# Kernel optimization log

Measured on AMD Instinct MI355X. Metric: run time of the kernel, lower is better.

## Reference

```python
import jax, jax.numpy as jnp
import numpy as np

N = 8192
D_IN = 512
D_OUT = 256
ALPHA = 0.2
NEG = -9e15


def setup_inputs() -> dict:
    key = jax.random.key(0)
    k1, k2, k3, k4 = jax.random.split(key, 4)
    node = jax.random.normal(k1, (N, D_IN), dtype=jnp.float32)
    adj = jax.random.randint(k2, (N, N), 0, 2, dtype=jnp.int32)
    # xavier_uniform with gain=1.414
    gain = 1.414
    lim_w = gain * np.sqrt(6.0 / (D_IN + D_OUT))
    weight = jax.random.uniform(k3, (D_IN, D_OUT), minval=-lim_w, maxval=lim_w, dtype=jnp.float32)
    lim_a = gain * np.sqrt(6.0 / (2 * D_OUT + 1))
    a = jax.random.uniform(k4, (2 * D_OUT, 1), minval=-lim_a, maxval=lim_a, dtype=jnp.float32)
    bias = jnp.zeros((D_OUT,), dtype=jnp.float32)
    return {"node": node, "adj": adj, "weight": weight, "a": a, "bias": bias}


def reference(node, adj, weight, a, bias):
    # v: [N, D_OUT]
    v = node @ weight
    # per-node attention scalars: Q, K are [N, 1]
    Q = v @ a[:D_OUT, :]
    K = v @ a[D_OUT:, :]
    e = jax.nn.leaky_relu(Q + K.T, negative_slope=ALPHA)  # [N, N]
    attention = jnp.where(adj > 0, e, NEG)
    attention = jax.nn.softmax(attention, axis=1)
    # dropout is identity in eval mode (self.training == False)
    out = attention @ v  # [N, D_OUT]
    out = jax.nn.leaky_relu(out, negative_slope=ALPHA)
    # F.normalize(p=2, dim=1): x / max(||x||_2, 1e-12)
    norm = jnp.linalg.norm(out, axis=1, keepdims=True)
    out = out / jnp.maximum(norm, 1e-12)
    return out + bias
```

## Files before the change

### kernel.cpp

```cpp
#include <hip/hip_runtime.h>
#include <hip/hip_bf16.h>

#define N_NODES 8192
#define DIN     512
#define DOUT    256
#define ALPHA   0.2f
#define LOG2E   1.4426950408889634f

typedef __bf16 bf16x8 __attribute__((ext_vector_type(8)));
typedef __bf16 bf16x4 __attribute__((ext_vector_type(4)));
typedef float  f32x4  __attribute__((ext_vector_type(4)));
typedef int    i32x4  __attribute__((ext_vector_type(4)));
typedef unsigned u32x4 __attribute__((ext_vector_type(4)));

__global__ __launch_bounds__(256) void k_repack_w(const float* __restrict__ w,
                                                  bf16x8* __restrict__ wB,
                                                  unsigned* __restrict__ kmaxkey) {
    if (blockIdx.x == 0 && threadIdx.x == 0) *kmaxkey = 0u;
    int u = blockIdx.x * 256 + threadIdx.x;
    int lane = u & 63, t = u >> 6;
    int nt = t & 15, kt = t >> 4;
    int k0 = kt * 32 + (lane >> 4) * 8;
    int col = nt * 16 + (lane & 15);
    bf16x8 r;
#pragma unroll
    for (int i = 0; i < 8; ++i) r[i] = (__bf16)w[(size_t)(k0 + i) * DOUT + col];
    wB[u] = r;
}

__global__ __launch_bounds__(256) void k_gemm1f(const float* __restrict__ node,
                                                const bf16x8* __restrict__ wB,
                                                const float* __restrict__ a,
                                                bf16x8* __restrict__ vBo,
                                                float* __restrict__ Q, float* __restrict__ K,
                                                unsigned* __restrict__ kmaxkey) {
    __shared__ __bf16 vsh[32][260];
    __shared__ float qksh[32][2];
    int lane = threadIdx.x & 63, w = threadIdx.x >> 6;
    int r15 = lane & 15, g = lane >> 4;
    int nh = w & 1, rh = w >> 1;
    int rowbase = blockIdx.x * 32;
    int myrow = rowbase + rh * 16 + r15;
    const float* np = node + (size_t)myrow * DIN + g * 8;

    f32x4 acc[8];
#pragma unroll
    for (int j = 0; j < 8; ++j) acc[j] = (f32x4){0.f, 0.f, 0.f, 0.f};

    f32x4 c0 = *(const f32x4*)np;
    f32x4 c1 = *(const f32x4*)(np + 4);
    f32x4 c2 = *(const f32x4*)(np + 32);
    f32x4 c3 = *(const f32x4*)(np + 36);
    const bf16x8* wp = wB + (size_t)(nh * 8) * 64 + lane;
    bf16x8 fr0 = wp[0], fr1 = wp[64], fr2 = wp[128], fr3 = wp[192];
    bf16x8 fr4 = wp[256], fr5 = wp[320], fr6 = wp[384], fr7 = wp[448];

    for (int kt = 0; kt < 16; ++kt) {
        f32x4 u0 = c0, u1 = c1;
        c0 = c2; c1 = c3;
        if (kt + 2 < 16) {
            c2 = *(const f32x4*)(np + (kt + 2) * 32);
            c3 = *(const f32x4*)(np + (kt + 2) * 32 + 4);
        }
        bf16x8 f0 = fr0, f1 = fr1, f2 = fr2, f3 = fr3;
        bf16x8 f4 = fr4, f5 = fr5, f6 = fr6, f7 = fr7;
        if (kt + 1 < 16) {
            const bf16x8* wn = wB + ((size_t)(kt + 1) * 16 + nh * 8) * 64 + lane;
            fr0 = wn[0]; fr1 = wn[64]; fr2 = wn[128]; fr3 = wn[192];
            fr4 = wn[256]; fr5 = wn[320]; fr6 = wn[384]; fr7 = wn[448];
        }
        bf16x8 af;
#pragma unroll
        for (int i = 0; i < 4; ++i) { af[i] = (__bf16)u0[i]; af[i + 4] = (__bf16)u1[i]; }
        acc[0] = __builtin_amdgcn_mfma_f32_16x16x32_bf16(af, f0, acc[0], 0, 0, 0);
        acc[1] = __builtin_amdgcn_mfma_f32_16x16x32_bf16(af, f1, acc[1], 0, 0, 0);
        acc[2] = __builtin_amdgcn_mfma_f32_16x16x32_bf16(af, f2, acc[2], 0, 0, 0);
        acc[3] = __builtin_amdgcn_mfma_f32_16x16x32_bf16(af, f3, acc[3], 0, 0, 0);
        acc[4] = __builtin_amdgcn_mfma_f32_16x16x32_bf16(af, f4, acc[4], 0, 0, 0);
        acc[5] = __builtin_amdgcn_mfma_f32_16x16x32_bf16(af, f5, acc[5], 0, 0, 0);
        acc[6] = __builtin_amdgcn_mfma_f32_16x16x32_bf16(af, f6, acc[6], 0, 0, 0);
        acc[7] = __builtin_amdgcn_mfma_f32_16x16x32_bf16(af, f7, acc[7], 0, 0, 0);
    }

    float qp0 = 0.f, qp1 = 0.f, qp2 = 0.f, qp3 = 0.f;
    float kp0 = 0.f, kp1 = 0.f, kp2 = 0.f, kp3 = 0.f;
#pragma unroll
    for (int j = 0; j < 8; ++j) {
        int col = (nh * 8 + j) * 16 + r15;
        float a1 = a[col], a2 = a[DOUT + col];
        qp0 += acc[j][0] * a1; qp1 += acc[j][1] * a1;
        qp2 += acc[j][2] * a1; qp3 += acc[j][3] * a1;
        kp0 += acc[j][0] * a2; kp1 += acc[j][1] * a2;
        kp2 += acc[j][2] * a2; kp3 += acc[j][3] * a2;
    }
#pragma unroll
    for (int m = 1; m < 16; m <<= 1) {
        qp0 += __shfl_xor(qp0, m); qp1 += __shfl_xor(qp1, m);
        qp2 += __shfl_xor(qp2, m); qp3 += __shfl_xor(qp3, m);
        kp0 += __shfl_xor(kp0, m); kp1 += __shfl_xor(kp1, m);
        kp2 += __shfl_xor(kp2, m); kp3 += __shfl_xor(kp3, m);
    }

#pragma unroll
    for (int j = 0; j < 8; ++j)
#pragma unroll
        for (int r = 0; r < 4; ++r)
            vsh[rh * 16 + g * 4 + r][(nh * 8 + j) * 16 + r15] = (__bf16)acc[j][r];
    if (nh == 0 && r15 == 0) {
        int rl = rh * 16 + g * 4;
        qksh[rl + 0][0] = qp0; qksh[rl + 1][0] = qp1; qksh[rl + 2][0] = qp2; qksh[rl + 3][0] = qp3;
        qksh[rl + 0][1] = kp0; qksh[rl + 1][1] = kp1; qksh[rl + 2][1] = kp2; qksh[rl + 3][1] = kp3;
    }
    __syncthreads();
    if (nh == 1 && r15 == 0) {
        int rl = rh * 16 + g * 4;
        int rw = rowbase + rl;
        float q0 = qp0 + qksh[rl + 0][0], q1 = qp1 + qksh[rl + 1][0];
        float q2 = qp2 + qksh[rl + 2][0], q3 = qp3 + qksh[rl + 3][0];
        float k0 = kp0 + qksh[rl + 0][1], k1 = kp1 + qksh[rl + 1][1];
        float k2 = kp2 + qksh[rl + 2][1], k3 = kp3 + qksh[rl + 3][1];
        Q[rw + 0] = q0; Q[rw + 1] = q1; Q[rw + 2] = q2; Q[rw + 3] = q3;
        K[rw + 0] = k0; K[rw + 1] = k1; K[rw + 2] = k2; K[rw + 3] = k3;
        float km = fmaxf(fmaxf(k0, k1), fmaxf(k2, k3));
        unsigned bits = __float_as_uint(km);
        unsigned key = (bits & 0x80000000u) ? ~bits : (bits | 0x80000000u);
        atomicMax(kmaxkey, key);
    }
#pragma unroll
    for (int uu = 0; uu < 4; ++uu) {
        int nt = w * 4 + uu;
        bf16x8 t;
#pragma unroll
        for (int i = 0; i < 8; ++i) t[i] = vsh[g * 8 + i][nt * 16 + r15];
        vBo[((size_t)blockIdx.x * 16 + nt) * 64 + lane] = t;
    }
}

template<int JS>
__global__ __launch_bounds__(256) void k_attn(const int* __restrict__ adj,
                                              const bf16x8* __restrict__ vBg,
                                              const float* __restrict__ Q,
                                              const float* __restrict__ K,
                                              const unsigned* __restrict__ kmaxkey,
                                              __bf16* __restrict__ accB,
                                              float* __restrict__ Sp) {
    constexpr int JR   = N_NODES / JS;
    constexpr int BIT  = JR / 32;
    constexpr int MSTR = BIT + 4;
    __shared__ float    Ks[JR];
    __shared__ unsigned Ms[64][MSTR];
    __shared__ bf16x8   pT[2][4][64];

    int bid = blockIdx.x;
    int rb = bid / JS, p = bid % JS;
    int lane = threadIdx.x & 63, w = threadIdx.x >> 6;
    int r15 = lane & 15, g = lane >> 4;
    int rowbase = rb * 64;
    int prow = rowbase + w * 16 + r15;
    int j0 = p * JR;

    for (int s = threadIdx.x * 4; s < JR; s += 1024)
        *(f32x4*)&Ks[s] = *(const f32x4*)&K[j0 + s];

    {
        const int t = threadIdx.x;
#pragma unroll
        for (int s = 0; s < BIT / 4; ++s) {
            int task = s * 256 + t;
            int row = task / BIT, dcol = task % BIT;
            const int* src = adj + (size_t)(rowbase + row) * N_NODES + j0 + dcol * 32;
            unsigned m = 0;
#pragma unroll
            for (int q = 0; q < 8; ++q) {
                i32x4 av = *(const i32x4*)(src + q * 4);
                m |= (av[0] != 0 ? 1u : 0u) << (q * 4 + 0);
                m |= (av[1] != 0 ? 1u : 0u) << (q * 4 + 1);
                m |= (av[2] != 0 ? 1u : 0u) << (q * 4 + 2);
                m |= (av[3] != 0 ? 1u : 0u) << (q * 4 + 3);
            }
            Ms[row][dcol] = m;
        }
    }

    float qi = Q[prow];
    unsigned kk = *kmaxkey;
    unsigned kb = (kk & 0x80000000u) ? (kk ^ 0x80000000u) : ~kk;
    float kmax = __uint_as_float(kb);
    float t0 = qi + kmax;
    float c2 = fmaxf(t0, ALPHA * t0) * LOG2E;

    const bf16x8* vbp = vBg + ((size_t)(p * BIT) * 16 + w * 4) * 64 + lane;

    f32x4 acc[4][4];
#pragma unroll
    for (int m = 0; m < 4; ++m)
#pragma unroll
        for (int n = 0; n < 4; ++n) acc[m][n] = (f32x4){0.f, 0.f, 0.f, 0.f};
    float sl = 0.f;

    __syncthreads();

    u32x4 Wc = *(const u32x4*)&Ms[w * 16 + r15][0];
    bf16x8 vS0 = vbp[0],    vS1 = vbp[64],   vS2 = vbp[128],  vS3 = vbp[192];
    bf16x8 vT0 = vbp[1024], vT1 = vbp[1088], vT2 = vbp[1152], vT3 = vbp[1216];

#define BODYM(W32, V0, V1, V2, V3, BUF, itv)                                    \
    {                                                                           \
        bf16x8 b0 = V0, b1 = V1, b2 = V2, b3 = V3;                              \
        if ((itv) + 2 < BIT) {                                                  \
            V0 = vbp[((itv) + 2) * 1024];       V1 = vbp[((itv) + 2) * 1024 + 64];  \
            V2 = vbp[((itv) + 2) * 1024 + 128]; V3 = vbp[((itv) + 2) * 1024 + 192]; \
        }                                                                       \
        f32x4 q0 = *(const f32x4*)&Ks[(itv) * 32 + g * 8];                      \
        f32x4 q1 = *(const f32x4*)&Ks[(itv) * 32 + g * 8 + 4];                  \
        unsigned wsh = (W32) >> (g * 8);                                        \
        bf16x8 af;                                                              \
        _Pragma("unroll")                                                       \
        for (int i = 0; i < 8; ++i) {                                           \
            float kj = (i < 4) ? q0[i] : q1[i - 4];                             \
            float tt = qi + kj;                                                 \
            float ft = fmaxf(tt, ALPHA * tt);                                   \
            float pv = __builtin_amdgcn_exp2f(ft * LOG2E - c2);                 \
            pv = (wsh & (1u << i)) ? pv : 0.f;                                  \
            sl += pv;                                                           \
            af[i] = (__bf16)pv;                                                 \
        }                                                                       \
        pT[BUF][w][lane] = af;                                                  \
        asm volatile("s_waitcnt lgkmcnt(0)" ::: "memory");                      \
        __builtin_amdgcn_s_barrier();                                           \
        asm volatile("" ::: "memory");                                          \
        bf16x8 pa0 = pT[BUF][0][lane], pa1 = pT[BUF][1][lane];                  \
        bf16x8 pa2 = pT[BUF][2][lane], pa3 = pT[BUF][3][lane];                  \
        acc[0][0] = __builtin_amdgcn_mfma_f32_16x16x32_bf16(pa0, b0, acc[0][0], 0, 0, 0); \
        acc[0][1] = __builtin_amdgcn_mfma_f32_16x16x32_bf16(pa0, b1, acc[0][1], 0, 0, 0); \
        acc[0][2] = __builtin_amdgcn_mfma_f32_16x16x32_bf16(pa0, b2, acc[0][2], 0, 0, 0); \
        acc[0][3] = __builtin_amdgcn_mfma_f32_16x16x32_bf16(pa0, b3, acc[0][3], 0, 0, 0); \
        acc[1][0] = __builtin_amdgcn_mfma_f32_16x16x32_bf16(pa1, b0, acc[1][0], 0, 0, 0); \
        acc[1][1] = __builtin_amdgcn_mfma_f32_16x16x32_bf16(pa1, b1, acc[1][1], 0, 0, 0); \
        acc[1][2] = __builtin_amdgcn_mfma_f32_16x16x32_bf16(pa1, b2, acc[1][2], 0, 0, 0); \
        acc[1][3] = __builtin_amdgcn_mfma_f32_16x16x32_bf16(pa1, b3, acc[1][3], 0, 0, 0); \
        acc[2][0] = __builtin_amdgcn_mfma_f32_16x16x32_bf16(pa2, b0, acc[2][0], 0, 0, 0); \
        acc[2][1] = __builtin_amdgcn_mfma_f32_16x16x32_bf16(pa2, b1, acc[2][1], 0, 0, 0); \
        acc[2][2] = __builtin_amdgcn_mfma_f32_16x16x32_bf16(pa2, b2, acc[2][2], 0, 0, 0); \
        acc[2][3] = __builtin_amdgcn_mfma_f32_16x16x32_bf16(pa2, b3, acc[2][3], 0, 0, 0); \
        acc[3][0] = __builtin_amdgcn_mfma_f32_16x16x32_bf16(pa3, b0, acc[3][0], 0, 0, 0); \
        acc[3][1] = __builtin_amdgcn_mfma_f32_16x16x32_bf16(pa3, b1, acc[3][1], 0, 0, 0); \
        acc[3][2] = __builtin_amdgcn_mfma_f32_16x16x32_bf16(pa3, b2, acc[3][2], 0, 0, 0); \
        acc[3][3] = __builtin_amdgcn_mfma_f32_16x16x32_bf16(pa3, b3, acc[3][3], 0, 0, 0); \
    }

    for (int it4 = 0; it4 < BIT; it4 += 4) {
        u32x4 Wn = Wc;
        if (it4 + 4 < BIT) Wn = *(const u32x4*)&Ms[w * 16 + r15][it4 + 4];
        BODYM(Wc[0], vS0, vS1, vS2, vS3, 0, it4 + 0)
        BODYM(Wc[1], vT0, vT1, vT2, vT3, 1, it4 + 1)
        BODYM(Wc[2], vS0, vS1, vS2, vS3, 0, it4 + 2)
        BODYM(Wc[3], vT0, vT1, vT2, vT3, 1, it4 + 3)
        Wc = Wn;
    }
#undef BODYM

    sl += __shfl_xor(sl, 16);
    sl += __shfl_xor(sl, 32);
    if (g == 0) Sp[(size_t)p * N_NODES + prow] = sl;

    __bf16* apb = accB + ((size_t)p * N_NODES + rowbase) * DOUT;
#pragma unroll
    for (int m = 0; m < 4; ++m)
#pragma unroll
        for (int r = 0; r < 4; ++r) {
            bf16x4 t;
#pragma unroll
            for (int n = 0; n < 4; ++n) t[n] = (__bf16)acc[m][n][r];
            *(bf16x4*)&apb[(size_t)(m * 16 + g * 4 + r) * DOUT + w * 64 + r15 * 4] = t;
        }
}

template<int JS>
__global__ __launch_bounds__(256) void k_final(const __bf16* __restrict__ accB,
                                               const float* __restrict__ Sp,
                                               const float* __restrict__ bias,
                                               float* __restrict__ out) {
    int lane = threadIdx.x & 63, wv = threadIdx.x >> 6;
    int row = blockIdx.x * 4 + wv;
    float s = 0.f;
    f32x4 av = (f32x4){0.f, 0.f, 0.f, 0.f};
#pragma unroll
    for (int pp = 0; pp < JS; ++pp) {
        bf16x4 t = *(const bf16x4*)&accB[((size_t)pp * N_NODES + row) * DOUT + lane * 4];
#pragma unroll
        for (int j = 0; j < 4; ++j) av[j] += (float)t[j];
        s += Sp[(size_t)pp * N_NODES + row];
    }
    float inv = 1.0f / fmaxf(s, 1e-30f);
    f32x4 o;
#pragma unroll
    for (int j = 0; j < 4; ++j) {
        float x = av[j] * inv;
        o[j] = fmaxf(x, ALPHA * x);
    }
    float sq = o[0] * o[0] + o[1] * o[1] + o[2] * o[2] + o[3] * o[3];
#pragma unroll
    for (int m = 1; m < 64; m <<= 1) sq += __shfl_xor(sq, m);
    float innrm = 1.0f / fmaxf(sqrtf(sq), 1e-12f);
#pragma unroll
    for (int j = 0; j < 4; ++j) {
        int col = (lane >> 4) * 64 + j * 16 + (lane & 15);
        out[(size_t)row * DOUT + col] = o[j] * innrm + bias[col];
    }
}

extern "C" void kernel_launch(void* const* d_in, const int* in_sizes, int n_in,
                              void* d_out, int out_size, void* d_ws, size_t ws_size,
                              hipStream_t stream) {
    const float* node   = (const float*)d_in[0];
    const int*   adj    = (const int*)d_in[1];
    const float* weight = (const float*)d_in[2];
    const float* a      = (const float*)d_in[3];
    const float* bias   = (const float*)d_in[4];
    float* out = (float*)d_out;

    const size_t fixed  = 4522240;
    const size_t per_js = 32768 + (size_t)N_NODES * DOUT * 2;
    int js = (ws_size >= fixed + 8 * per_js) ? 8 : 4;

    char* ws = (char*)d_ws;
    bf16x8*   wB      = (bf16x8*)(ws);
    bf16x8*   vB      = (bf16x8*)(ws + 262144);
    float*    Q       = (float*)(ws + 4456448);
    float*    K       = (float*)(ws + 4489216);
    unsigned* kmaxkey = (unsigned*)(ws + 4521984);
    float*    Sp      = (float*)(ws + fixed);
    __bf16*   accB    = (__bf16*)(ws + fixed + (size_t)js * 32768);

    k_repack_w<<<dim3(64),  dim3(256), 0, stream>>>(weight, wB, kmaxkey);
    k_gemm1f  <<<dim3(256), dim3(256), 0, stream>>>(node, wB, a, vB, Q, K, kmaxkey);
    if (js == 8) {
        k_attn<8><<<dim3(128 * 8), dim3(256), 0, stream>>>(adj, vB, Q, K, kmaxkey, accB, Sp);
        k_final<8><<<dim3(2048), dim3(256), 0, stream>>>(accB, Sp, bias, out);
    } else {
        k_attn<4><<<dim3(128 * 4), dim3(256), 0, stream>>>(adj, vB, Q, K, kmaxkey, accB, Sp);
        k_final<4><<<dim3(2048), dim3(256), 0, stream>>>(accB, Sp, bias, out);
    }
}
```

Baseline: 138.6 us.

## Stream adjacency bitmask packing into the attention main loop and simplify exp math

Instead of loading and packing the whole adjacency block into a shared-memory bitmask before the main loop, the kernel now packs only the first two column groups up front. Later groups are loaded and packed inside the loop two groups ahead, so the large int32 adjacency reads overlap with the exp and MFMA work. The leaky-relu plus exp argument is rewritten as a max of two FMAs with precomputed constants. Launch bounds now request two blocks per CU. This adds register pressure from the in-flight adjacency vectors, and the packing is only correct if NG is at least 3 and matches the four-threads-per-row mapping.

```diff
diff --git a/kernel.cpp b/kernel.cpp
--- a/kernel.cpp
+++ b/kernel.cpp
@@ -137,15 +137,16 @@
 }
 
 template<int JS>
-__global__ __launch_bounds__(256) void k_attn(const int* __restrict__ adj,
-                                              const bf16x8* __restrict__ vBg,
-                                              const float* __restrict__ Q,
-                                              const float* __restrict__ K,
-                                              const unsigned* __restrict__ kmaxkey,
-                                              __bf16* __restrict__ accB,
-                                              float* __restrict__ Sp) {
+__global__ __launch_bounds__(256, 2) void k_attn(const int* __restrict__ adj,
+                                                 const bf16x8* __restrict__ vBg,
+                                                 const float* __restrict__ Q,
+                                                 const float* __restrict__ K,
+                                                 const unsigned* __restrict__ kmaxkey,
+                                                 __bf16* __restrict__ accB,
+                                                 float* __restrict__ Sp) {
     constexpr int JR   = N_NODES / JS;
     constexpr int BIT  = JR / 32;
+    constexpr int NG   = BIT / 4;
     constexpr int MSTR = BIT + 4;
     __shared__ float    Ks[JR];
     __shared__ unsigned Ms[64][MSTR];
@@ -162,25 +163,28 @@
     for (int s = threadIdx.x * 4; s < JR; s += 1024)
         *(f32x4*)&Ks[s] = *(const f32x4*)&K[j0 + s];
 
+    const int t = threadIdx.x;
+    const int mrow = t >> 2, msub = t & 3;
+    const int* abase = adj + (size_t)(rowbase + mrow) * N_NODES + j0;
+
+#define ISSUE8(L, DC) { const int* src_ = abase + (DC) * 32;                     \
+    _Pragma("unroll") for (int q = 0; q < 8; ++q) L[q] = *(const i32x4*)(src_ + q * 4); }
+#define PACK32(L) ({ unsigned m_ = 0u;                                           \
+    _Pragma("unroll") for (int q = 0; q < 8; ++q) {                              \
+        m_ |= (L[q][0] != 0 ? 1u : 0u) << (q * 4 + 0);                           \
+        m_ |= (L[q][1] != 0 ? 1u : 0u) << (q * 4 + 1);                           \
+        m_ |= (L[q][2] != 0 ? 1u : 0u) << (q * 4 + 2);                           \
+        m_ |= (L[q][3] != 0 ? 1u : 0u) << (q * 4 + 3); } m_; })
+
+    i32x4 La[8];
     {
-        const int t = threadIdx.x;
-#pragma unroll
-        for (int s = 0; s < BIT / 4; ++s) {
-            int task = s * 256 + t;
-            int row = task / BIT, dcol = task % BIT;
-            const int* src = adj + (size_t)(rowbase + row) * N_NODES + j0 + dcol * 32;
-            unsigned m = 0;
-#pragma unroll
-            for (int q = 0; q < 8; ++q) {
-                i32x4 av = *(const i32x4*)(src + q * 4);
-                m |= (av[0] != 0 ? 1u : 0u) << (q * 4 + 0);
-                m |= (av[1] != 0 ? 1u : 0u) << (q * 4 + 1);
-                m |= (av[2] != 0 ? 1u : 0u) << (q * 4 + 2);
-                m |= (av[3] != 0 ? 1u : 0u) << (q * 4 + 3);
-            }
-            Ms[row][dcol] = m;
-        }
-    }
+        i32x4 Lb[8];
+        ISSUE8(La, msub)
+        ISSUE8(Lb, 4 + msub)
+        Ms[mrow][msub] = PACK32(La);
+        Ms[mrow][4 + msub] = PACK32(Lb);
+    }
+    ISSUE8(La, 8 + msub)
 
     float qi = Q[prow];
     unsigned kk = *kmaxkey;
@@ -188,6 +192,9 @@
     float kmax = __uint_as_float(kb);
     float t0 = qi + kmax;
     float c2 = fmaxf(t0, ALPHA * t0) * LOG2E;
+    float qiL = qi * LOG2E;
+    float A1 = qiL - c2;
+    float A2 = ALPHA * qiL - c2;
 
     const bf16x8* vbp = vBg + ((size_t)(p * BIT) * 16 + w * 4) * 64 + lane;
 
@@ -198,7 +205,9 @@
         for (int n = 0; n < 4; ++n) acc[m][n] = (f32x4){0.f, 0.f, 0.f, 0.f};
     float sl = 0.f;
 
-    __syncthreads();
+    asm volatile("s_waitcnt lgkmcnt(0)" ::: "memory");
+    __builtin_amdgcn_s_barrier();
+    asm volatile("" ::: "memory");
 
     u32x4 Wc = *(const u32x4*)&Ms[w * 16 + r15][0];
     bf16x8 vS0 = vbp[0],    vS1 = vbp[64],   vS2 = vbp[128],  vS3 = vbp[192];
@@ -218,9 +227,9 @@
         _Pragma("unroll")                                                       \
         for (int i = 0; i < 8; ++i) {                                           \
             float kj = (i < 4) ? q0[i] : q1[i - 4];                             \
-            float tt = qi + kj;                                                 \
-            float ft = fmaxf(tt, ALPHA * tt);                                   \
-            float pv = __builtin_amdgcn_exp2f(ft * LOG2E - c2);                 \
+            float f1 = __builtin_fmaf(kj, LOG2E, A1);                           \
+            float f2 = __builtin_fmaf(kj, ALPHA * LOG2E, A2);                   \
+            float pv = __builtin_amdgcn_exp2f(fmaxf(f1, f2));                   \
             pv = (wsh & (1u << i)) ? pv : 0.f;                                  \
             sl += pv;                                                           \
             af[i] = (__bf16)pv;                                                 \
@@ -228,7 +237,7 @@
         pT[BUF][w][lane] = af;                                                  \
         asm volatile("s_waitcnt lgkmcnt(0)" ::: "memory");                      \
         __builtin_amdgcn_s_barrier();                                           \
-        asm volatile("" ::: "memory");                                          \
+        asm volatile("" ::: "memory");                                         \
         bf16x8 pa0 = pT[BUF][0][lane], pa1 = pT[BUF][1][lane];                  \
         bf16x8 pa2 = pT[BUF][2][lane], pa3 = pT[BUF][3][lane];                  \
         acc[0][0] = __builtin_amdgcn_mfma_f32_16x16x32_bf16(pa0, b0, acc[0][0], 0, 0, 0); \
@@ -249,16 +258,23 @@
         acc[3][3] = __builtin_amdgcn_mfma_f32_16x16x32_bf16(pa3, b3, acc[3][3], 0, 0, 0); \
     }
 
-    for (int it4 = 0; it4 < BIT; it4 += 4) {
+    for (int G = 0; G < NG; ++G) {
+        const int it4 = G * 4;
         u32x4 Wn = Wc;
-        if (it4 + 4 < BIT) Wn = *(const u32x4*)&Ms[w * 16 + r15][it4 + 4];
+        if (G + 1 < NG) Wn = *(const u32x4*)&Ms[w * 16 + r15][it4 + 4];
         BODYM(Wc[0], vS0, vS1, vS2, vS3, 0, it4 + 0)
         BODYM(Wc[1], vT0, vT1, vT2, vT3, 1, it4 + 1)
+        if (G + 2 < NG) {
+            Ms[mrow][(G + 2) * 4 + msub] = PACK32(La);
+            if (G + 3 < NG) ISSUE8(La, (G + 3) * 4 + msub)
+        }
         BODYM(Wc[2], vS0, vS1, vS2, vS3, 0, it4 + 2)
         BODYM(Wc[3], vT0, vT1, vT2, vT3, 1, it4 + 3)
         Wc = Wn;
     }
 #undef BODYM
+#undef ISSUE8
+#undef PACK32
 
     sl += __shfl_xor(sl, 16);
     sl += __shfl_xor(sl, 32);
@@ -269,10 +285,10 @@
     for (int m = 0; m < 4; ++m)
 #pragma unroll
         for (int r = 0; r < 4; ++r) {
-            bf16x4 t;
-#pragma unroll
-            for (int n = 0; n < 4; ++n) t[n] = (__bf16)acc[m][n][r];
-            *(bf16x4*)&apb[(size_t)(m * 16 + g * 4 + r) * DOUT + w * 64 + r15 * 4] = t;
+            bf16x4 t2;
+#pragma unroll
+            for (int n = 0; n < 4; ++n) t2[n] = (__bf16)acc[m][n][r];
+            *(bf16x4*)&apb[(size_t)(m * 16 + g * 4 + r) * DOUT + w * 64 + r15 * 4] = t2;
         }
 }
 
```

New measurement: 122.1 us. 1.14x faster.

## Restructure attention kernel: async adj staging to LDS, per-wave rows, no P exchange

Applied to the files above, without the earlier changes.

Replaces the attention kernel so each block handles 128 rows and each wave owns 32 full rows across all 256 output columns. The per-iteration LDS exchange of probabilities and its barrier are removed. The adjacency matrix is no longer pre-packed into bitmasks. Raw int rows are streamed into double-buffered, XOR-swizzled LDS with global_load_lds, overlapping the next chunk's load with the current MFMAs. The exponent is rewritten as two FMAs plus a max, and the output store layout is changed, with the final kernel's column mapping updated to match. The cost is larger register accumulators (occupancy bound 2) and more LDS traffic for the unpacked mask.

```diff
diff --git a/kernel.cpp b/kernel.cpp
--- a/kernel.cpp
+++ b/kernel.cpp
@@ -11,7 +11,14 @@
 typedef __bf16 bf16x4 __attribute__((ext_vector_type(4)));
 typedef float  f32x4  __attribute__((ext_vector_type(4)));
 typedef int    i32x4  __attribute__((ext_vector_type(4)));
-typedef unsigned u32x4 __attribute__((ext_vector_type(4)));
+
+#define MFMA16 __builtin_amdgcn_mfma_f32_16x16x32_bf16
+
+__device__ __forceinline__ void gld16(const int* g, int* l) {
+    __builtin_amdgcn_global_load_lds(
+        (const __attribute__((address_space(1))) void*)g,
+        (__attribute__((address_space(3))) void*)l, 16, 0, 0);
+}
 
 __global__ __launch_bounds__(256) void k_repack_w(const float* __restrict__ w,
                                                   bf16x8* __restrict__ wB,
@@ -72,14 +79,14 @@
         bf16x8 af;
 #pragma unroll
         for (int i = 0; i < 4; ++i) { af[i] = (__bf16)u0[i]; af[i + 4] = (__bf16)u1[i]; }
-        acc[0] = __builtin_amdgcn_mfma_f32_16x16x32_bf16(af, f0, acc[0], 0, 0, 0);
-        acc[1] = __builtin_amdgcn_mfma_f32_16x16x32_bf16(af, f1, acc[1], 0, 0, 0);
-        acc[2] = __builtin_amdgcn_mfma_f32_16x16x32_bf16(af, f2, acc[2], 0, 0, 0);
-        acc[3] = __builtin_amdgcn_mfma_f32_16x16x32_bf16(af, f3, acc[3], 0, 0, 0);
-        acc[4] = __builtin_amdgcn_mfma_f32_16x16x32_bf16(af, f4, acc[4], 0, 0, 0);
-        acc[5] = __builtin_amdgcn_mfma_f32_16x16x32_bf16(af, f5, acc[5], 0, 0, 0);
-        acc[6] = __builtin_amdgcn_mfma_f32_16x16x32_bf16(af, f6, acc[6], 0, 0, 0);
-        acc[7] = __builtin_amdgcn_mfma_f32_16x16x32_bf16(af, f7, acc[7], 0, 0, 0);
+        acc[0] = MFMA16(af, f0, acc[0], 0, 0, 0);
+        acc[1] = MFMA16(af, f1, acc[1], 0, 0, 0);
+        acc[2] = MFMA16(af, f2, acc[2], 0, 0, 0);
+        acc[3] = MFMA16(af, f3, acc[3], 0, 0, 0);
+        acc[4] = MFMA16(af, f4, acc[4], 0, 0, 0);
+        acc[5] = MFMA16(af, f5, acc[5], 0, 0, 0);
+        acc[6] = MFMA16(af, f6, acc[6], 0, 0, 0);
+        acc[7] = MFMA16(af, f7, acc[7], 0, 0, 0);
     }
 
     float qp0 = 0.f, qp1 = 0.f, qp2 = 0.f, qp3 = 0.f;
@@ -137,143 +144,151 @@
 }
 
 template<int JS>
-__global__ __launch_bounds__(256) void k_attn(const int* __restrict__ adj,
-                                              const bf16x8* __restrict__ vBg,
-                                              const float* __restrict__ Q,
-                                              const float* __restrict__ K,
-                                              const unsigned* __restrict__ kmaxkey,
-                                              __bf16* __restrict__ accB,
-                                              float* __restrict__ Sp) {
-    constexpr int JR   = N_NODES / JS;
-    constexpr int BIT  = JR / 32;
-    constexpr int MSTR = BIT + 4;
-    __shared__ float    Ks[JR];
-    __shared__ unsigned Ms[64][MSTR];
-    __shared__ bf16x8   pT[2][4][64];
-
-    int bid = blockIdx.x;
-    int rb = bid / JS, p = bid % JS;
-    int lane = threadIdx.x & 63, w = threadIdx.x >> 6;
-    int r15 = lane & 15, g = lane >> 4;
-    int rowbase = rb * 64;
-    int prow = rowbase + w * 16 + r15;
-    int j0 = p * JR;
+__global__ __launch_bounds__(256, 2) void k_attn2(const int* __restrict__ adj,
+                                                  const bf16x8* __restrict__ vBg,
+                                                  const float* __restrict__ Q,
+                                                  const float* __restrict__ K,
+                                                  const unsigned* __restrict__ kmaxkey,
+                                                  __bf16* __restrict__ accB,
+                                                  float* __restrict__ Sp) {
+    constexpr int JR  = N_NODES / JS;
+    constexpr int BIT = JR / 32;
+    constexpr int NCH = JR / 64;
+    __shared__ float Ks[JR];
+    __shared__ int   Ar[2][4][2048];
+
+    const int bid = blockIdx.x;
+    const int rb = bid / JS, p = bid % JS;
+    const int lane = threadIdx.x & 63, w = threadIdx.x >> 6;
+    const int r15 = lane & 15, g = lane >> 4;
+    const int rowbase = rb * 128;
+    const int prow0 = rowbase + w * 32 + r15;
+    const int j0 = p * JR;
 
     for (int s = threadIdx.x * 4; s < JR; s += 1024)
         *(f32x4*)&Ks[s] = *(const f32x4*)&K[j0 + s];
 
-    {
-        const int t = threadIdx.x;
-#pragma unroll
-        for (int s = 0; s < BIT / 4; ++s) {
-            int task = s * 256 + t;
-            int row = task / BIT, dcol = task % BIT;
-            const int* src = adj + (size_t)(rowbase + row) * N_NODES + j0 + dcol * 32;
-            unsigned m = 0;
-#pragma unroll
-            for (int q = 0; q < 8; ++q) {
-                i32x4 av = *(const i32x4*)(src + q * 4);
-                m |= (av[0] != 0 ? 1u : 0u) << (q * 4 + 0);
-                m |= (av[1] != 0 ? 1u : 0u) << (q * 4 + 1);
-                m |= (av[2] != 0 ? 1u : 0u) << (q * 4 + 2);
-                m |= (av[3] != 0 ? 1u : 0u) << (q * 4 + 3);
-            }
-            Ms[row][dcol] = m;
-        }
-    }
-
-    float qi = Q[prow];
+    const int* rlane = adj + (size_t)(rowbase + w * 32 + (lane >> 4)) * N_NODES + j0;
+    const int colE = 4 * ((lane & 15) ^ (lane >> 4));
+    const int colO = 4 * ((lane & 15) ^ (4 + (lane >> 4)));
+
+#define STAGE(c) { const int* gp_ = rlane + (c) * 64; int* lp_ = &Ar[(c) & 1][w][0];  \
+    _Pragma("unroll") for (int t_ = 0; t_ < 8; ++t_)                                  \
+        gld16(gp_ + (size_t)t_ * 4 * N_NODES + ((t_ & 1) ? colO : colE), lp_ + t_ * 256); }
+
+    STAGE(0)
+
+    float qi0 = Q[prow0], qi1 = Q[prow0 + 16];
     unsigned kk = *kmaxkey;
     unsigned kb = (kk & 0x80000000u) ? (kk ^ 0x80000000u) : ~kk;
     float kmax = __uint_as_float(kb);
-    float t0 = qi + kmax;
-    float c2 = fmaxf(t0, ALPHA * t0) * LOG2E;
-
-    const bf16x8* vbp = vBg + ((size_t)(p * BIT) * 16 + w * 4) * 64 + lane;
-
-    f32x4 acc[4][4];
-#pragma unroll
-    for (int m = 0; m < 4; ++m)
-#pragma unroll
-        for (int n = 0; n < 4; ++n) acc[m][n] = (f32x4){0.f, 0.f, 0.f, 0.f};
-    float sl = 0.f;
+    float t00 = qi0 + kmax, t01 = qi1 + kmax;
+    float c20 = fmaxf(t00, ALPHA * t00) * LOG2E;
+    float c21 = fmaxf(t01, ALPHA * t01) * LOG2E;
+    float A10 = qi0 * LOG2E - c20, A20 = ALPHA * qi0 * LOG2E - c20;
+    float A11 = qi1 * LOG2E - c21, A21 = ALPHA * qi1 * LOG2E - c21;
+
+    f32x4 ac0[16], ac1[16];
+#pragma unroll
+    for (int nt = 0; nt < 16; ++nt) {
+        ac0[nt] = (f32x4){0.f, 0.f, 0.f, 0.f};
+        ac1[nt] = (f32x4){0.f, 0.f, 0.f, 0.f};
+    }
+    float sl0 = 0.f, sl1 = 0.f;
 
     __syncthreads();
 
-    u32x4 Wc = *(const u32x4*)&Ms[w * 16 + r15][0];
-    bf16x8 vS0 = vbp[0],    vS1 = vbp[64],   vS2 = vbp[128],  vS3 = vbp[192];
-    bf16x8 vT0 = vbp[1024], vT1 = vbp[1088], vT2 = vbp[1152], vT3 = vbp[1216];
-
-#define BODYM(W32, V0, V1, V2, V3, BUF, itv)                                    \
-    {                                                                           \
-        bf16x8 b0 = V0, b1 = V1, b2 = V2, b3 = V3;                              \
-        if ((itv) + 2 < BIT) {                                                  \
-            V0 = vbp[((itv) + 2) * 1024];       V1 = vbp[((itv) + 2) * 1024 + 64];  \
-            V2 = vbp[((itv) + 2) * 1024 + 128]; V3 = vbp[((itv) + 2) * 1024 + 192]; \
-        }                                                                       \
-        f32x4 q0 = *(const f32x4*)&Ks[(itv) * 32 + g * 8];                      \
-        f32x4 q1 = *(const f32x4*)&Ks[(itv) * 32 + g * 8 + 4];                  \
-        unsigned wsh = (W32) >> (g * 8);                                        \
-        bf16x8 af;                                                              \
-        _Pragma("unroll")                                                       \
-        for (int i = 0; i < 8; ++i) {                                           \
-            float kj = (i < 4) ? q0[i] : q1[i - 4];                             \
-            float tt = qi + kj;                                                 \
-            float ft = fmaxf(tt, ALPHA * tt);                                   \
-            float pv = __builtin_amdgcn_exp2f(ft * LOG2E - c2);                 \
-            pv = (wsh & (1u << i)) ? pv : 0.f;                                  \
-            sl += pv;                                                           \
-            af[i] = (__bf16)pv;                                                 \
-        }                                                                       \
-        pT[BUF][w][lane] = af;                                                  \
-        asm volatile("s_waitcnt lgkmcnt(0)" ::: "memory");                      \
-        __builtin_amdgcn_s_barrier();                                           \
-        asm volatile("" ::: "memory");                                          \
-        bf16x8 pa0 = pT[BUF][0][lane], pa1 = pT[BUF][1][lane];                  \
-        bf16x8 pa2 = pT[BUF][2][lane], pa3 = pT[BUF][3][lane];                  \
-        acc[0][0] = __builtin_amdgcn_mfma_f32_16x16x32_bf16(pa0, b0, acc[0][0], 0, 0, 0); \
-        acc[0][1] = __builtin_amdgcn_mfma_f32_16x16x32_bf16(pa0, b1, acc[0][1], 0, 0, 0); \
-        acc[0][2] = __builtin_amdgcn_mfma_f32_16x16x32_bf16(pa0, b2, acc[0][2], 0, 0, 0); \
-        acc[0][3] = __builtin_amdgcn_mfma_f32_16x16x32_bf16(pa0, b3, acc[0][3], 0, 0, 0); \
-        acc[1][0] = __builtin_amdgcn_mfma_f32_16x16x32_bf16(pa1, b0, acc[1][0], 0, 0, 0); \
-        acc[1][1] = __builtin_amdgcn_mfma_f32_16x16x32_bf16(pa1, b1, acc[1][1], 0, 0, 0); \
-        acc[1][2] = __builtin_amdgcn_mfma_f32_16x16x32_bf16(pa1, b2, acc[1][2], 0, 0, 0); \
-        acc[1][3] = __builtin_amdgcn_mfma_f32_16x16x32_bf16(pa1, b3, acc[1][3], 0, 0, 0); \
-        acc[2][0] = __builtin_amdgcn_mfma_f32_16x16x32_bf16(pa2, b0, acc[2][0], 0, 0, 0); \
-        acc[2][1] = __builtin_amdgcn_mfma_f32_16x16x32_bf16(pa2, b1, acc[2][1], 0, 0, 0); \
-        acc[2][2] = __builtin_amdgcn_mfma_f32_16x16x32_bf16(pa2, b2, acc[2][2], 0, 0, 0); \
-        acc[2][3] = __builtin_amdgcn_mfma_f32_16x16x32_bf16(pa2, b3, acc[2][3], 0, 0, 0); \
-        acc[3][0] = __builtin_amdgcn_mfma_f32_16x16x32_bf16(pa3, b0, acc[3][0], 0, 0, 0); \
-        acc[3][1] = __builtin_amdgcn_mfma_f32_16x16x32_bf16(pa3, b1, acc[3][1], 0, 0, 0); \
-        acc[3][2] = __builtin_amdgcn_mfma_f32_16x16x32_bf16(pa3, b2, acc[3][2], 0, 0, 0); \
-        acc[3][3] = __builtin_amdgcn_mfma_f32_16x16x32_bf16(pa3, b3, acc[3][3], 0, 0, 0); \
-    }
-
-    for (int it4 = 0; it4 < BIT; it4 += 4) {
-        u32x4 Wn = Wc;
-        if (it4 + 4 < BIT) Wn = *(const u32x4*)&Ms[w * 16 + r15][it4 + 4];
-        BODYM(Wc[0], vS0, vS1, vS2, vS3, 0, it4 + 0)
-        BODYM(Wc[1], vT0, vT1, vT2, vT3, 1, it4 + 1)
-        BODYM(Wc[2], vS0, vS1, vS2, vS3, 0, it4 + 2)
-        BODYM(Wc[3], vT0, vT1, vT2, vT3, 1, it4 + 3)
-        Wc = Wn;
-    }
-#undef BODYM
-
-    sl += __shfl_xor(sl, 16);
-    sl += __shfl_xor(sl, 32);
-    if (g == 0) Sp[(size_t)p * N_NODES + prow] = sl;
-
-    __bf16* apb = accB + ((size_t)p * N_NODES + rowbase) * DOUT;
-#pragma unroll
-    for (int m = 0; m < 4; ++m)
-#pragma unroll
-        for (int r = 0; r < 4; ++r) {
-            bf16x4 t;
-#pragma unroll
-            for (int n = 0; n < 4; ++n) t[n] = (__bf16)acc[m][n][r];
-            *(bf16x4*)&apb[(size_t)(m * 16 + g * 4 + r) * DOUT + w * 64 + r15 * 4] = t;
-        }
+    const bf16x8* vbp = vBg + (size_t)(p * (JR >> 5)) * 1024 + lane;
+
+    for (int itv = 0; itv < BIT; ++itv) {
+        if ((itv & 3) == 0 && itv) __builtin_amdgcn_s_barrier();
+
+        const bf16x8* vs = vbp + (size_t)itv * 1024;
+        bf16x8 B0[8];
+#pragma unroll
+        for (int nt = 0; nt < 8; ++nt) B0[nt] = vs[nt * 64];
+
+        f32x4 q0 = *(const f32x4*)&Ks[itv * 32 + g * 8];
+        f32x4 q1 = *(const f32x4*)&Ks[itv * 32 + g * 8 + 4];
+        const int* ap = &Ar[(itv >> 1) & 1][w][0];
+        const int hh = (itv & 1) << 5;
+
+        bf16x8 af0, af1;
+        {
+            int o = ((r15 * 64) + hh + (g << 3)) ^ ((r15 & 7) << 2);
+            i32x4 a0 = *(const i32x4*)(ap + o);
+            i32x4 a1 = *(const i32x4*)(ap + (o ^ 4));
+#pragma unroll
+            for (int i = 0; i < 8; ++i) {
+                float kj = (i < 4) ? q0[i] : q1[i - 4];
+                float f1 = __builtin_fmaf(kj, LOG2E, A10);
+                float f2 = __builtin_fmaf(kj, ALPHA * LOG2E, A20);
+                float pv = __builtin_amdgcn_exp2f(fmaxf(f1, f2));
+                int av = (i < 4) ? a0[i] : a1[i - 4];
+                pv = av ? pv : 0.f;
+                sl0 += pv; af0[i] = (__bf16)pv;
+            }
+        }
+        {
+            int o = (((r15 + 16) * 64) + hh + (g << 3)) ^ ((r15 & 7) << 2);
+            i32x4 a0 = *(const i32x4*)(ap + o);
+            i32x4 a1 = *(const i32x4*)(ap + (o ^ 4));
+#pragma unroll
+            for (int i = 0; i < 8; ++i) {
+                float kj = (i < 4) ? q0[i] : q1[i - 4];
+                float f1 = __builtin_fmaf(kj, LOG2E, A11);
+                float f2 = __builtin_fmaf(kj, ALPHA * LOG2E, A21);
+                float pv = __builtin_amdgcn_exp2f(fmaxf(f1, f2));
+                int av = (i < 4) ? a0[i] : a1[i - 4];
+                pv = av ? pv : 0.f;
+                sl1 += pv; af1[i] = (__bf16)pv;
+            }
+        }
+
+        bf16x8 B1[8];
+#pragma unroll
+        for (int nt = 0; nt < 8; ++nt) B1[nt] = vs[(nt + 8) * 64];
+
+        if (!(itv & 1)) {
+            int c = (itv >> 1) + 1;
+            if (c < NCH) { STAGE(c) }
+            __builtin_amdgcn_sched_barrier(0);
+        }
+
+#pragma unroll
+        for (int nt = 0; nt < 8; ++nt) {
+            ac0[nt] = MFMA16(af0, B0[nt], ac0[nt], 0, 0, 0);
+            ac1[nt] = MFMA16(af1, B0[nt], ac1[nt], 0, 0, 0);
+        }
+#pragma unroll
+        for (int nt = 0; nt < 8; ++nt) {
+            ac0[nt + 8] = MFMA16(af0, B1[nt], ac0[nt + 8], 0, 0, 0);
+            ac1[nt + 8] = MFMA16(af1, B1[nt], ac1[nt + 8], 0, 0, 0);
+        }
+    }
+#undef STAGE
+
+    sl0 += __shfl_xor(sl0, 16); sl0 += __shfl_xor(sl0, 32);
+    sl1 += __shfl_xor(sl1, 16); sl1 += __shfl_xor(sl1, 32);
+    if (lane < 16) {
+        Sp[(size_t)p * N_NODES + prow0] = sl0;
+        Sp[(size_t)p * N_NODES + prow0 + 16] = sl1;
+    }
+
+    __bf16* apb = accB + ((size_t)p * N_NODES + rowbase + w * 32) * DOUT;
+#pragma unroll
+    for (int reg = 0; reg < 4; ++reg) {
+        bf16x8 s0, s1, s2, s3;
+#pragma unroll
+        for (int nt = 0; nt < 8; ++nt) {
+            s0[nt] = (__bf16)ac0[nt][reg];     s1[nt] = (__bf16)ac0[nt + 8][reg];
+            s2[nt] = (__bf16)ac1[nt][reg];     s3[nt] = (__bf16)ac1[nt + 8][reg];
+        }
+        size_t r0 = (size_t)(g * 4 + reg) * DOUT + r15 * 16;
+        size_t r1 = (size_t)(16 + g * 4 + reg) * DOUT + r15 * 16;
+        *(bf16x8*)&apb[r0] = s0;     *(bf16x8*)&apb[r0 + 8] = s1;
+        *(bf16x8*)&apb[r1] = s2;     *(bf16x8*)&apb[r1 + 8] = s3;
+    }
 }
 
 template<int JS>
@@ -305,7 +320,7 @@
     float innrm = 1.0f / fmaxf(sqrtf(sq), 1e-12f);
 #pragma unroll
     for (int j = 0; j < 4; ++j) {
-        int col = (lane >> 4) * 64 + j * 16 + (lane & 15);
+        int col = ((lane & 3) * 4 + j) * 16 + (lane >> 2);
         out[(size_t)row * DOUT + col] = o[j] * innrm + bias[col];
     }
 }
@@ -336,10 +351,10 @@
     k_repack_w<<<dim3(64),  dim3(256), 0, stream>>>(weight, wB, kmaxkey);
     k_gemm1f  <<<dim3(256), dim3(256), 0, stream>>>(node, wB, a, vB, Q, K, kmaxkey);
     if (js == 8) {
-        k_attn<8><<<dim3(128 * 8), dim3(256), 0, stream>>>(adj, vB, Q, K, kmaxkey, accB, Sp);
+        k_attn2<8><<<dim3(64 * 8), dim3(256), 0, stream>>>(adj, vB, Q, K, kmaxkey, accB, Sp);
         k_final<8><<<dim3(2048), dim3(256), 0, stream>>>(accB, Sp, bias, out);
     } else {
-        k_attn<4><<<dim3(128 * 4), dim3(256), 0, stream>>>(adj, vB, Q, K, kmaxkey, accB, Sp);
+        k_attn2<4><<<dim3(64 * 4), dim3(256), 0, stream>>>(adj, vB, Q, K, kmaxkey, accB, Sp);
         k_final<4><<<dim3(2048), dim3(256), 0, stream>>>(accB, Sp, bias, out);
     }
 }
```

After: 120.4 us. 1.15x faster.
